# Kernel optimization log

Measured on AMD Instinct MI355X. Metric: run time of the kernel, lower is better.

Reference implementation:

```python
import jax, jax.numpy as jnp
import numpy as np

STATE_DIM = 128
N_STATES = 4096
N_ACTIONS = 512
D = 16384  # random_feature_dim
B = 16     # batch of parallel episodes
ALPHA = 1.0
BETA = 1.0
SQRT_D = np.sqrt(D).astype(np.float32)


def _phi(W, x):
    """RandomFeatureMap: exp(1j * W @ x / alpha) / sqrt(D).
    W: [D, state_dim] real (torch randn .to(complex64) has zero imag part).
    x: [..., state_dim] real -> returns complex64 [..., D].
    """
    z = jnp.einsum('di,...i->...d', W, x) / ALPHA  # real phase
    return jax.lax.complex(jnp.cos(z), jnp.sin(z)) / SQRT_D


def setup_inputs() -> dict:
    key = jax.random.key(0)
    k1, k2, k3, k4, k5 = jax.random.split(key, 5)
    obs = jax.random.uniform(k1, (B, N_STATES), dtype=jnp.float32)
    action = jax.random.uniform(k2, (B, N_ACTIONS), dtype=jnp.float32)
    Q = jax.random.normal(k3, (STATE_DIM, N_STATES), dtype=jnp.float32) / np.sqrt(STATE_DIM).astype(np.float32)
    V = jax.random.normal(k4, (STATE_DIM, N_ACTIONS), dtype=jnp.float32) / np.sqrt(STATE_DIM).astype(np.float32)
    W = jax.random.normal(k5, (D, STATE_DIM), dtype=jnp.float32) / ALPHA
    return {"obs": obs, "action": action, "Q": Q, "V": V, "W": W}


def reference(obs, action, Q, V, W):
    # phi_Q = random_feature_map(Q.T).T : [D, n_states], also the memory M
    phi_Q = _phi(W, Q.T).T                                  # [D, S] complex64
    # get_state_from_memory: state = M @ obs
    state = phi_Q @ obs.T.astype(jnp.complex64)             # [D, B]
    # clean_up: weights = softmax(beta * Re(phi_Q^H @ state)); new_state = phi_Q @ weights
    scores = BETA * jnp.real(phi_Q.conj().T @ state)        # [S, B]
    weights = jax.nn.softmax(scores, axis=0)
    new_state = phi_Q @ weights.astype(jnp.complex64)       # [D, B]
    # update_state: state *= phi(V @ action)
    v = V @ action.T                                        # [state_dim, B]
    phi_v = _phi(W, v.T).T                                  # [D, B]
    out_state = new_state * phi_v
    # get_obs_from_memory: softmax(beta * Re(M^H @ state))
    out_scores = jax.nn.softmax(BETA * jnp.real(phi_Q.conj().T @ out_state), axis=0)  # [S, B]
    return out_scores
```

## Files before the change

kernel.cpp:

```cpp
#include <hip/hip_runtime.h>
#include <hip/hip_bf16.h>
#include <cstdint>
#include <cstddef>

#define D_DIM 16384
#define S_DIM 4096
#define A_DIM 512
#define K_DIM 128
#define B_DIM 16

#define INV2PI 0.15915494309189535f

typedef float f32x4 __attribute__((ext_vector_type(4)));
typedef short s16x8 __attribute__((ext_vector_type(8)));
typedef unsigned short u16;
typedef unsigned int   u32;

__device__ __forceinline__ u16 bf16bits(float x) {
    return __builtin_bit_cast(u16, (__bf16)x);
}
__device__ __forceinline__ s16x8 frag_cast(uint4 u) {
    return __builtin_bit_cast(s16x8, u);
}
__device__ __forceinline__ u32 cvt_pk_bf16(float lo, float hi) {
    u32 r;
    asm("v_cvt_pk_bf16_f32 %0, %1, %2" : "=v"(r) : "v"(lo), "v"(hi));
    return r;
}
__device__ __forceinline__ int sigma(int row) {
    return (row & 7) ^ ((row >> 1) & 4);
}
__device__ __forceinline__ void g2l16(const u32* g, u32* l) {
    __builtin_amdgcn_global_load_lds((const __attribute__((address_space(1))) u32*)g,
                                     (__attribute__((address_space(3))) u32*)l, 16, 0, 0);
}

__global__ void prep_kernel(const float* __restrict__ W, const float* __restrict__ Q,
                            const float* __restrict__ obs,
                            u16* __restrict__ Wb, u16* __restrict__ QT, u16* __restrict__ obsP)
{
    const int i0 = blockIdx.x * 256 + threadIdx.x;
    const int stride = gridDim.x * 256;
    const float4* wp = (const float4*)W;
    for (int i = i0; i < D_DIM * 16; i += stride) {
        float4 a = wp[2 * i], b = wp[2 * i + 1];
        uint4 o;
        o.x = cvt_pk_bf16(a.x * INV2PI, a.y * INV2PI);
        o.y = cvt_pk_bf16(a.z * INV2PI, a.w * INV2PI);
        o.z = cvt_pk_bf16(b.x * INV2PI, b.y * INV2PI);
        o.w = cvt_pk_bf16(b.z * INV2PI, b.w * INV2PI);
        ((uint4*)Wb)[i] = o;
    }
    for (int i = i0; i < S_DIM * 16; i += stride) {
        const int s = i >> 4, kc = i & 15;
        float q[8];
        #pragma unroll
        for (int j = 0; j < 8; ++j) q[j] = Q[(size_t)(kc * 8 + j) * S_DIM + s];
        uint4 o;
        o.x = cvt_pk_bf16(q[0], q[1]);
        o.y = cvt_pk_bf16(q[2], q[3]);
        o.z = cvt_pk_bf16(q[4], q[5]);
        o.w = cvt_pk_bf16(q[6], q[7]);
        ((uint4*)QT)[s * 16 + kc] = o;
    }
    for (int i = i0; i < B_DIM * S_DIM; i += stride) {
        int b = i >> 12, s = i & 4095;
        obsP[((s >> 3) << 7) + (b << 3) + (s & 7)] = bf16bits(obs[i]);
    }
}

__global__ void kv_kernel(const float* __restrict__ V, const float* __restrict__ act,
                          float* __restrict__ v)
{
    const int t = threadIdx.x;
    const int out = blockIdx.x * 32 + (t >> 3);
    const int part = t & 7;
    const int k = out >> 4, b = out & 15;
    const float4* vp = (const float4*)(V + (size_t)k * A_DIM);
    const float4* ap = (const float4*)(act + (size_t)b * A_DIM);
    float s = 0.f;
    #pragma unroll
    for (int q = part * 16; q < part * 16 + 16; ++q) {
        float4 x = vp[q], y = ap[q];
        s += x.x * y.x + x.y * y.y + x.z * y.z + x.w * y.w;
    }
    s += __shfl_xor(s, 1, 64);
    s += __shfl_xor(s, 2, 64);
    s += __shfl_xor(s, 4, 64);
    if (part == 0) v[out] = s;
}

__global__ void phiv_kernel(const float* __restrict__ W, const float* __restrict__ v,
                            float* __restrict__ pvr, float* __restrict__ pvi)
{
    __shared__ float sv[K_DIM * 16];
    const int tid = threadIdx.x;
    for (int j = tid; j < K_DIM * 16; j += 256) sv[j] = v[j];
    __syncthreads();
    const int i = blockIdx.x * 256 + tid;
    const int d = i >> 4, b = i & 15;
    const float4* wp = (const float4*)(W + (size_t)d * K_DIM);
    float z = 0.f;
    #pragma unroll 8
    for (int q = 0; q < 32; ++q) {
        float4 w4 = wp[q];
        z += w4.x * sv[(4 * q + 0) * 16 + b] + w4.y * sv[(4 * q + 1) * 16 + b]
           + w4.z * sv[(4 * q + 2) * 16 + b] + w4.w * sv[(4 * q + 3) * 16 + b];
    }
    pvr[i] = cosf(z) * 0.0078125f;
    pvi[i] = sinf(z) * 0.0078125f;
}

template<int MODE>
__global__ __launch_bounds__(256, 4)
void fused_pass(const u16* __restrict__ P1, const u16* __restrict__ P2,
                const u16* __restrict__ y1, const u16* __restrict__ y2,
                float* __restrict__ out1, float* __restrict__ out2, int Mrows)
{
    __shared__ u32 lds[2][4096];
    const int tid = threadIdx.x;
    const int w   = tid >> 6;
    const int l   = tid & 63;
    const int n0  = l & 15;
    const int hi  = l >> 4;
    const int wm  = w & 1;
    const int wk  = w >> 1;
    const int m0  = blockIdx.x * 64 + wm * 32;
    const int kbase0 = blockIdx.y * 512;

    s16x8 bfrag[2][4];
    #pragma unroll
    for (int mt = 0; mt < 2; ++mt) {
        const uint4* ap = (const uint4*)(P1 + (size_t)(m0 + 16 * mt + n0) * 128);
        #pragma unroll
        for (int ki = 0; ki < 4; ++ki) bfrag[mt][ki] = frag_cast(ap[4 * ki + hi]);
    }

    int gofs[4];
    #pragma unroll
    for (int i = 0; i < 4; ++i) {
        const int row = 16 * w + 4 * i + (l >> 4);
        gofs[i] = row * 128 + (((l & 15) ^ sigma(row)) << 3);
    }
    const u16* p2base = P2 + (size_t)kbase0 * 128;

    f32x4 acc1[2] = {{0.f,0.f,0.f,0.f},{0.f,0.f,0.f,0.f}};
    f32x4 acc2[2] = {{0.f,0.f,0.f,0.f},{0.f,0.f,0.f,0.f}};

    const int rowT0 = 32 * wk + 8 * (n0 >> 2) + (n0 & 3);

    {
        const u16* src = p2base;
        #pragma unroll
        for (int i = 0; i < 4; ++i)
            g2l16((const u32*)(src + gofs[i]), &lds[0][w * 1024 + i * 256]);
    }
    __syncthreads();

    #pragma unroll 1
    for (int c = 0; c < 8; ++c) {
        if (c < 7) {
            const u16* src = p2base + (size_t)(c + 1) * 64 * 128;
            #pragma unroll
            for (int i = 0; i < 4; ++i)
                g2l16((const u32*)(src + gofs[i]), &lds[(c + 1) & 1][w * 1024 + i * 256]);
        }
        const int kbase = kbase0 + c * 64;
        const u32* buf = lds[c & 1];
        u32 cf[2][4], sf[2][4];
        #pragma unroll
        for (int T = 0; T < 2; ++T) {
            const int row = rowT0 + 4 * T;
            const int sg  = sigma(row);
            const u32* rb = buf + row * 64;
            uint4 af[4];
            #pragma unroll
            for (int ki = 0; ki < 4; ++ki)
                af[ki] = *(const uint4*)(rb + (((4 * ki + hi) ^ sg) << 2));
            f32x4 z0 = {0.f,0.f,0.f,0.f}, z1 = {0.f,0.f,0.f,0.f};
            #pragma unroll
            for (int ki = 0; ki < 4; ++ki) {
                z0 = __builtin_amdgcn_mfma_f32_16x16x32_bf16(frag_cast(af[ki]), bfrag[0][ki], z0, 0, 0, 0);
                z1 = __builtin_amdgcn_mfma_f32_16x16x32_bf16(frag_cast(af[ki]), bfrag[1][ki], z1, 0, 0, 0);
            }
            float c0[4], s0[4], c1[4], s1[4];
            #pragma unroll
            for (int r = 0; r < 4; ++r) {
                const float rv0 = __builtin_amdgcn_fractf(z0[r]);
                c0[r] = __builtin_amdgcn_cosf(rv0);
                s0[r] = __builtin_amdgcn_sinf(rv0);
                const float rv1 = __builtin_amdgcn_fractf(z1[r]);
                c1[r] = __builtin_amdgcn_cosf(rv1);
                s1[r] = __builtin_amdgcn_sinf(rv1);
            }
            cf[0][2 * T + 0] = cvt_pk_bf16(c0[0], c0[1]);
            cf[0][2 * T + 1] = cvt_pk_bf16(c0[2], c0[3]);
            sf[0][2 * T + 0] = cvt_pk_bf16(s0[0], s0[1]);
            sf[0][2 * T + 1] = cvt_pk_bf16(s0[2], s0[3]);
            cf[1][2 * T + 0] = cvt_pk_bf16(c1[0], c1[1]);
            cf[1][2 * T + 1] = cvt_pk_bf16(c1[2], c1[3]);
            sf[1][2 * T + 0] = cvt_pk_bf16(s1[0], s1[1]);
            sf[1][2 * T + 1] = cvt_pk_bf16(s1[2], s1[3]);
        }
        const size_t yg = (size_t)((kbase >> 3) + 4 * wk + hi) * 128 + (size_t)n0 * 8;
        const s16x8 yf1 = frag_cast(*(const uint4*)(y1 + yg));
        if (MODE == 0) {
            #pragma unroll
            for (int mt = 0; mt < 2; ++mt) {
                acc1[mt] = __builtin_amdgcn_mfma_f32_16x16x32_bf16(
                    frag_cast(uint4{cf[mt][0], cf[mt][1], cf[mt][2], cf[mt][3]}), yf1, acc1[mt], 0, 0, 0);
                acc2[mt] = __builtin_amdgcn_mfma_f32_16x16x32_bf16(
                    frag_cast(uint4{sf[mt][0], sf[mt][1], sf[mt][2], sf[mt][3]}), yf1, acc2[mt], 0, 0, 0);
            }
        } else {
            const s16x8 yf2 = frag_cast(*(const uint4*)(y2 + yg));
            #pragma unroll
            for (int mt = 0; mt < 2; ++mt) {
                acc1[mt] = __builtin_amdgcn_mfma_f32_16x16x32_bf16(
                    frag_cast(uint4{cf[mt][0], cf[mt][1], cf[mt][2], cf[mt][3]}), yf1, acc1[mt], 0, 0, 0);
                acc1[mt] = __builtin_amdgcn_mfma_f32_16x16x32_bf16(
                    frag_cast(uint4{sf[mt][0], sf[mt][1], sf[mt][2], sf[mt][3]}), yf2, acc1[mt], 0, 0, 0);
            }
        }
        __syncthreads();
    }

    float* red = reinterpret_cast<float*>(&lds[0][0]);
    if (wk == 1) {
        #pragma unroll
        for (int mt = 0; mt < 2; ++mt)
            #pragma unroll
            for (int r = 0; r < 4; ++r) {
                red[((wm * 2 + mt) * 16 + 4 * hi + r) * 16 + n0] = acc1[mt][r];
                if (MODE == 0)
                    red[1024 + ((wm * 2 + mt) * 16 + 4 * hi + r) * 16 + n0] = acc2[mt][r];
            }
    }
    __syncthreads();
    if (wk == 0) {
        float* o1 = out1 + (size_t)blockIdx.y * Mrows * 16;
        float* o2 = out2 + (size_t)blockIdx.y * Mrows * 16;
        #pragma unroll
        for (int mt = 0; mt < 2; ++mt)
            #pragma unroll
            for (int r = 0; r < 4; ++r) {
                const int orow = m0 + 16 * mt + 4 * hi + r;
                const float v1 = acc1[mt][r] + red[((wm * 2 + mt) * 16 + 4 * hi + r) * 16 + n0];
                if (MODE == 0) {
                    o1[orow * 16 + n0] = v1;
                    o2[orow * 16 + n0] = acc2[mt][r] + red[1024 + ((wm * 2 + mt) * 16 + 4 * hi + r) * 16 + n0];
                } else {
                    o1[(size_t)n0 * Mrows + orow] = v1;
                }
            }
    }
}

__global__ void finishA(const float* __restrict__ ar, const float* __restrict__ ai,
                        u16* __restrict__ pr, u16* __restrict__ pi)
{
    const int i = blockIdx.x * 256 + threadIdx.x;
    float sr = 0.f, si = 0.f;
    #pragma unroll
    for (int p = 0; p < 8; ++p) {
        sr += ar[(size_t)p * (D_DIM * 16) + i];
        si += ai[(size_t)p * (D_DIM * 16) + i];
    }
    const int d = i >> 4, b = i & 15;
    const int pidx = ((d >> 3) << 7) + (b << 3) + (d & 7);
    pr[pidx] = bf16bits(sr * 0.0078125f);
    pi[pidx] = bf16bits(si * 0.0078125f);
}

__global__ void finishC(const float* __restrict__ ar, const float* __restrict__ ai,
                        const float* __restrict__ pvr, const float* __restrict__ pvi,
                        u16* __restrict__ pr, u16* __restrict__ pi)
{
    const int i = blockIdx.x * 256 + threadIdx.x;
    float sr = 0.f, si = 0.f;
    #pragma unroll
    for (int p = 0; p < 8; ++p) {
        sr += ar[(size_t)p * (D_DIM * 16) + i];
        si += ai[(size_t)p * (D_DIM * 16) + i];
    }
    const float nr = sr * 0.0078125f, ni = si * 0.0078125f;
    const float xr = nr * pvr[i] - ni * pvi[i];
    const float xi = nr * pvi[i] + ni * pvr[i];
    const int d = i >> 4, b = i & 15;
    const int pidx = ((d >> 3) << 7) + (b << 3) + (d & 7);
    pr[pidx] = bf16bits(xr);
    pi[pidx] = bf16bits(xi);
}

__global__ void reduce_scores(const float* __restrict__ acc, float* __restrict__ scT)
{
    const int i = blockIdx.x * 256 + threadIdx.x;
    float s = 0.f;
    #pragma unroll
    for (int p = 0; p < 32; ++p)
        s += acc[(size_t)p * (S_DIM * 16) + i];
    scT[i] = s * 0.0078125f;
}

template<int OUT>
__global__ void softmax_col(const float* __restrict__ scT, u16* __restrict__ wp,
                            float* __restrict__ outp)
{
    const int b = blockIdx.x;
    const int tid = threadIdx.x;
    __shared__ float red[4];
    const float4* src = (const float4*)(scT + (size_t)b * S_DIM);
    float4 x[4];
    float m = -1e30f;
    #pragma unroll
    for (int j = 0; j < 4; ++j) {
        x[j] = src[j * 256 + tid];
        m = fmaxf(fmaxf(m, fmaxf(x[j].x, x[j].y)), fmaxf(x[j].z, x[j].w));
    }
    #pragma unroll
    for (int off = 1; off < 64; off <<= 1) m = fmaxf(m, __shfl_xor(m, off, 64));
    if ((tid & 63) == 0) red[tid >> 6] = m;
    __syncthreads();
    m = fmaxf(fmaxf(red[0], red[1]), fmaxf(red[2], red[3]));
    float sum = 0.f;
    #pragma unroll
    for (int j = 0; j < 4; ++j) {
        x[j].x = expf(x[j].x - m); x[j].y = expf(x[j].y - m);
        x[j].z = expf(x[j].z - m); x[j].w = expf(x[j].w - m);
        sum += x[j].x + x[j].y + x[j].z + x[j].w;
    }
    #pragma unroll
    for (int off = 1; off < 64; off <<= 1) sum += __shfl_xor(sum, off, 64);
    __syncthreads();
    if ((tid & 63) == 0) red[tid >> 6] = sum;
    __syncthreads();
    const float inv = 1.0f / (red[0] + red[1] + red[2] + red[3]);
    #pragma unroll
    for (int j = 0; j < 4; ++j) {
        const int s4 = (j * 256 + tid) * 4;
        float v4[4] = {x[j].x * inv, x[j].y * inv, x[j].z * inv, x[j].w * inv};
        #pragma unroll
        for (int q = 0; q < 4; ++q) {
            const int s = s4 + q;
            if (OUT == 0) wp[((s >> 3) << 7) + (b << 3) + (s & 7)] = bf16bits(v4[q]);
            else          outp[s * 16 + b] = v4[q];
        }
    }
}

extern "C" void kernel_launch(void* const* d_in, const int* in_sizes, int n_in,
                              void* d_out, int out_size, void* d_ws, size_t ws_size,
                              hipStream_t stream)
{
    const float* obs = (const float*)d_in[0];
    const float* act = (const float*)d_in[1];
    const float* Q   = (const float*)d_in[2];
    const float* V   = (const float*)d_in[3];
    const float* W   = (const float*)d_in[4];
    float* out = (float*)d_out;
    char* ws = (char*)d_ws;

    u16*   Wb     = (u16*)  (ws + 0);
    u16*   QT     = (u16*)  (ws + 4194304);
    u16*   obsP   = (u16*)  (ws + 5242880);
    u16*   wP     = (u16*)  (ws + 5373952);
    u16*   stRe   = (u16*)  (ws + 5505024);
    u16*   stIm   = (u16*)  (ws + 6029312);
    u16*   osRe   = (u16*)  (ws + 6553600);
    u16*   osIm   = (u16*)  (ws + 7077888);
    float* pvR    = (float*)(ws + 7602176);
    float* pvI    = (float*)(ws + 8650752);
    float* vv     = (float*)(ws + 9699328);
    float* partR  = (float*)(ws + 9707520);
    float* partI  = (float*)(ws + 18096128);
    float* partS  = (float*)(ws + 9707520);
    float* scT    = (float*)(ws + 18096128);

    prep_kernel<<<1024, 256, 0, stream>>>(W, Q, obs, Wb, QT, obsP);
    kv_kernel<<<64, 256, 0, stream>>>(V, act, vv);
    phiv_kernel<<<1024, 256, 0, stream>>>(W, vv, pvR, pvI);

    fused_pass<0><<<dim3(256, 8), 256, 0, stream>>>(Wb, QT, obsP, obsP, partR, partI, D_DIM);
    finishA<<<1024, 256, 0, stream>>>(partR, partI, stRe, stIm);

    fused_pass<1><<<dim3(64, 32), 256, 0, stream>>>(QT, Wb, stRe, stIm, partS, partS, S_DIM);
    reduce_scores<<<256, 256, 0, stream>>>(partS, scT);
    softmax_col<0><<<16, 256, 0, stream>>>(scT, wP, nullptr);

    fused_pass<0><<<dim3(256, 8), 256, 0, stream>>>(Wb, QT, wP, wP, partR, partI, D_DIM);
    finishC<<<1024, 256, 0, stream>>>(partR, partI, pvR, pvI, osRe, osIm);

    fused_pass<1><<<dim3(64, 32), 256, 0, stream>>>(QT, Wb, osRe, osIm, partS, partS, S_DIM);
    reduce_scores<<<256, 256, 0, stream>>>(partS, scT);
    softmax_col<1><<<16, 256, 0, stream>>>(scT, nullptr, out);
}
```

Before: 234.8 us.

## Double split-K chunk length, prefetch y fragments, fuse score reduction into softmax

New measurement: 227.6 us. 1.03x faster.

```diff
diff --git a/kernel.cpp b/kernel.cpp
--- a/kernel.cpp
+++ b/kernel.cpp
@@ -8,6 +8,7 @@
 #define A_DIM 512
 #define K_DIM 128
 #define B_DIM 16
+#define CH    16
 
 #define INV2PI 0.15915494309189535f
 
@@ -126,7 +127,7 @@
     const int wm  = w & 1;
     const int wk  = w >> 1;
     const int m0  = blockIdx.x * 64 + wm * 32;
-    const int kbase0 = blockIdx.y * 512;
+    const int kbase0 = blockIdx.y * (CH * 64);
 
     s16x8 bfrag[2][4];
     #pragma unroll
@@ -149,23 +150,31 @@
 
     const int rowT0 = 32 * wk + 8 * (n0 >> 2) + (n0 & 3);
 
+    const size_t ybase = (size_t)(4 * wk + hi) * 128 + (size_t)n0 * 8;
+    #define YLD(Y, c) (*(const uint4*)((Y) + (size_t)((kbase0 + (c) * 64) >> 3) * 128 + ybase))
+
     {
         const u16* src = p2base;
         #pragma unroll
         for (int i = 0; i < 4; ++i)
             g2l16((const u32*)(src + gofs[i]), &lds[0][w * 1024 + i * 256]);
     }
+    uint4 y1c = YLD(y1, 0);
+    uint4 y2c;
+    if (MODE == 1) y2c = YLD(y2, 0);
     __syncthreads();
 
     #pragma unroll 1
-    for (int c = 0; c < 8; ++c) {
-        if (c < 7) {
+    for (int c = 0; c < CH; ++c) {
+        uint4 y1n, y2n;
+        if (c < CH - 1) {
             const u16* src = p2base + (size_t)(c + 1) * 64 * 128;
             #pragma unroll
             for (int i = 0; i < 4; ++i)
                 g2l16((const u32*)(src + gofs[i]), &lds[(c + 1) & 1][w * 1024 + i * 256]);
-        }
-        const int kbase = kbase0 + c * 64;
+            y1n = YLD(y1, c + 1);
+            if (MODE == 1) y2n = YLD(y2, c + 1);
+        }
         const u32* buf = lds[c & 1];
         u32 cf[2][4], sf[2][4];
         #pragma unroll
@@ -202,8 +211,7 @@
             sf[1][2 * T + 0] = cvt_pk_bf16(s1[0], s1[1]);
             sf[1][2 * T + 1] = cvt_pk_bf16(s1[2], s1[3]);
         }
-        const size_t yg = (size_t)((kbase >> 3) + 4 * wk + hi) * 128 + (size_t)n0 * 8;
-        const s16x8 yf1 = frag_cast(*(const uint4*)(y1 + yg));
+        const s16x8 yf1 = frag_cast(y1c);
         if (MODE == 0) {
             #pragma unroll
             for (int mt = 0; mt < 2; ++mt) {
@@ -213,7 +221,7 @@
                     frag_cast(uint4{sf[mt][0], sf[mt][1], sf[mt][2], sf[mt][3]}), yf1, acc2[mt], 0, 0, 0);
             }
         } else {
-            const s16x8 yf2 = frag_cast(*(const uint4*)(y2 + yg));
+            const s16x8 yf2 = frag_cast(y2c);
             #pragma unroll
             for (int mt = 0; mt < 2; ++mt) {
                 acc1[mt] = __builtin_amdgcn_mfma_f32_16x16x32_bf16(
@@ -223,7 +231,12 @@
             }
         }
         __syncthreads();
-    }
+        if (c < CH - 1) {
+            y1c = y1n;
+            if (MODE == 1) y2c = y2n;
+        }
+    }
+    #undef YLD
 
     float* red = reinterpret_cast<float*>(&lds[0][0]);
     if (wk == 1) {
@@ -262,7 +275,7 @@
     const int i = blockIdx.x * 256 + threadIdx.x;
     float sr = 0.f, si = 0.f;
     #pragma unroll
-    for (int p = 0; p < 8; ++p) {
+    for (int p = 0; p < 4; ++p) {
         sr += ar[(size_t)p * (D_DIM * 16) + i];
         si += ai[(size_t)p * (D_DIM * 16) + i];
     }
@@ -279,7 +292,7 @@
     const int i = blockIdx.x * 256 + threadIdx.x;
     float sr = 0.f, si = 0.f;
     #pragma unroll
-    for (int p = 0; p < 8; ++p) {
+    for (int p = 0; p < 4; ++p) {
         sr += ar[(size_t)p * (D_DIM * 16) + i];
         si += ai[(size_t)p * (D_DIM * 16) + i];
     }
@@ -292,29 +305,26 @@
     pi[pidx] = bf16bits(xi);
 }
 
-__global__ void reduce_scores(const float* __restrict__ acc, float* __restrict__ scT)
-{
-    const int i = blockIdx.x * 256 + threadIdx.x;
-    float s = 0.f;
-    #pragma unroll
-    for (int p = 0; p < 32; ++p)
-        s += acc[(size_t)p * (S_DIM * 16) + i];
-    scT[i] = s * 0.0078125f;
-}
-
 template<int OUT>
-__global__ void softmax_col(const float* __restrict__ scT, u16* __restrict__ wp,
+__global__ void softmax_col(const float* __restrict__ acc, u16* __restrict__ wp,
                             float* __restrict__ outp)
 {
     const int b = blockIdx.x;
     const int tid = threadIdx.x;
     __shared__ float red[4];
-    const float4* src = (const float4*)(scT + (size_t)b * S_DIM);
     float4 x[4];
     float m = -1e30f;
     #pragma unroll
     for (int j = 0; j < 4; ++j) {
-        x[j] = src[j * 256 + tid];
+        float4 s4 = {0.f, 0.f, 0.f, 0.f};
+        #pragma unroll
+        for (int p = 0; p < 16; ++p) {
+            const float4 t = *(const float4*)(acc + (size_t)p * (S_DIM * 16)
+                                              + (size_t)b * S_DIM + (j * 256 + tid) * 4);
+            s4.x += t.x; s4.y += t.y; s4.z += t.z; s4.w += t.w;
+        }
+        x[j].x = s4.x * 0.0078125f; x[j].y = s4.y * 0.0078125f;
+        x[j].z = s4.z * 0.0078125f; x[j].w = s4.w * 0.0078125f;
         m = fmaxf(fmaxf(m, fmaxf(x[j].x, x[j].y)), fmaxf(x[j].z, x[j].w));
     }
     #pragma unroll
@@ -337,11 +347,11 @@
     const float inv = 1.0f / (red[0] + red[1] + red[2] + red[3]);
     #pragma unroll
     for (int j = 0; j < 4; ++j) {
-        const int s4 = (j * 256 + tid) * 4;
+        const int s4i = (j * 256 + tid) * 4;
         float v4[4] = {x[j].x * inv, x[j].y * inv, x[j].z * inv, x[j].w * inv};
         #pragma unroll
         for (int q = 0; q < 4; ++q) {
-            const int s = s4 + q;
+            const int s = s4i + q;
             if (OUT == 0) wp[((s >> 3) << 7) + (b << 3) + (s & 7)] = bf16bits(v4[q]);
             else          outp[s * 16 + b] = v4[q];
         }
@@ -374,23 +384,20 @@
     float* partR  = (float*)(ws + 9707520);
     float* partI  = (float*)(ws + 18096128);
     float* partS  = (float*)(ws + 9707520);
-    float* scT    = (float*)(ws + 18096128);
 
     prep_kernel<<<1024, 256, 0, stream>>>(W, Q, obs, Wb, QT, obsP);
     kv_kernel<<<64, 256, 0, stream>>>(V, act, vv);
     phiv_kernel<<<1024, 256, 0, stream>>>(W, vv, pvR, pvI);
 
-    fused_pass<0><<<dim3(256, 8), 256, 0, stream>>>(Wb, QT, obsP, obsP, partR, partI, D_DIM);
+    fused_pass<0><<<dim3(256, 4), 256, 0, stream>>>(Wb, QT, obsP, obsP, partR, partI, D_DIM);
     finishA<<<1024, 256, 0, stream>>>(partR, partI, stRe, stIm);
 
-    fused_pass<1><<<dim3(64, 32), 256, 0, stream>>>(QT, Wb, stRe, stIm, partS, partS, S_DIM);
-    reduce_scores<<<256, 256, 0, stream>>>(partS, scT);
-    softmax_col<0><<<16, 256, 0, stream>>>(scT, wP, nullptr);
-
-    fused_pass<0><<<dim3(256, 8), 256, 0, stream>>>(Wb, QT, wP, wP, partR, partI, D_DIM);
+    fused_pass<1><<<dim3(64, 16), 256, 0, stream>>>(QT, Wb, stRe, stIm, partS, partS, S_DIM);
+    softmax_col<0><<<16, 256, 0, stream>>>(partS, wP, nullptr);
+
+    fused_pass<0><<<dim3(256, 4), 256, 0, stream>>>(Wb, QT, wP, wP, partR, partI, D_DIM);
     finishC<<<1024, 256, 0, stream>>>(partR, partI, pvR, pvI, osRe, osIm);
 
-    fused_pass<1><<<dim3(64, 32), 256, 0, stream>>>(QT, Wb, osRe, osIm, partS, partS, S_DIM);
-    reduce_scores<<<256, 256, 0, stream>>>(partS, scT);
-    softmax_col<1><<<16, 256, 0, stream>>>(scT, nullptr, out);
-}
+    fused_pass<1><<<dim3(64, 16), 256, 0, stream>>>(QT, Wb, osRe, osIm, partS, partS, S_DIM);
+    softmax_col<1><<<16, 256, 0, stream>>>(partS, nullptr, out);
+}
```
